# Optimization experiments

Hardware: AMD Instinct MI355X
Metric: run time of the kernel (lower is better)

Reference implementation:

```python
import jax, jax.numpy as jnp
import numpy as np
import math

TAU = 0.5        # module stores self.tau = 1.0 / tau with tau=2.0
THRESHOLD = 1.0
SURR_C = 1.0 / (2.0 * math.sqrt(2.0 * math.pi))  # coefficient in Stochastic.backward


@jax.custom_vjp
def spike(v):
    # Stochastic.forward: (input > 0).float()
    return (v > 0).astype(v.dtype)


def _spike_fwd(v):
    return spike(v), v


def _spike_bwd(v, g):
    # Stochastic.backward: grad * 1/(2*sqrt(2*pi)) * exp(-v^2/2)
    return (g * (SURR_C * jnp.exp(-0.5 * v * v)),)


spike.defvjp(_spike_fwd, _spike_bwd)


def setup_inputs() -> dict:
    key = jax.random.key(0)
    x = jax.random.normal(key, (32, 128, 8192), dtype=jnp.float32)  # [B, T, N]
    return {"x": x}


def reference(x):
    # Eval-mode iterative stochastic-LIF update (no noise injection).
    xt = jnp.swapaxes(x, 0, 1)  # [T, B, N] for scan over time

    def step(u, x_t):
        u = TAU * u + x_t                # leaky integrate
        o = spike(u - THRESHOLD)         # fire
        u = u * (1.0 - o)                # hard reset by multiply
        return u, o

    u0 = jnp.zeros_like(xt[0])
    _, o = jax.lax.scan(step, u0, xt)
    return jnp.swapaxes(o, 0, 1)  # [B, T, N]
```

## Files before the change

kernel.cpp:

```cpp
#include <hip/hip_runtime.h>
#include <stdint.h>


constexpr int B  = 32;
constexpr int T  = 128;
constexpr int N  = 8192;
constexpr int N4 = N / 4;
constexpr int THREADS = 128;
constexpr int SPAN4   = THREADS;
constexpr int NTILES  = N4 / SPAN4;
constexpr int DP      = 16;
constexpr int NG      = T / DP;

typedef float v4f __attribute__((ext_vector_type(4)));

__device__ __forceinline__ float lif1(float& u, float x) {
    u = 0.5f * u + x;
    const bool s = u > 1.0f;
    const float o = s ? 1.0f : 0.0f;
    u = s ? 0.0f : u;
    return o;
}

__device__ __forceinline__ void nt_store4(const float4& o, float4* p) {
    __builtin_nontemporal_store(*(const v4f*)&o, (v4f*)p);
}

__global__ __launch_bounds__(THREADS) void lif_kernel(const float4* __restrict__ x,
                                                      float4* __restrict__ out) {
    const int tid   = threadIdx.x;
    const int b     = blockIdx.x >> 4;
    const int ntile = blockIdx.x & (NTILES - 1);
    const uint32_t base4 = (uint32_t)b * (T * N4) + (uint32_t)ntile * SPAN4 + tid;
    const float4* gx = x + base4;
    float4*       go = out + base4;

    float4 pipe[DP];
    #pragma unroll
    for (int k = 0; k < DP; ++k) pipe[k] = gx[(uint32_t)k * N4];

    float ux = 0.f, uy = 0.f, uz = 0.f, uw = 0.f;

    #pragma unroll 1
    for (int g = 0; g < NG - 1; ++g) {
        const uint32_t roff = (uint32_t)(g + 1) * (DP * N4);
        const uint32_t woff = (uint32_t)g * (DP * N4);
        #pragma unroll
        for (int k = 0; k < DP; ++k) {
            const float4 v = pipe[k];
            pipe[k] = gx[roff + (uint32_t)k * N4];
            float4 o;
            o.x = lif1(ux, v.x);
            o.y = lif1(uy, v.y);
            o.z = lif1(uz, v.z);
            o.w = lif1(uw, v.w);
            nt_store4(o, go + woff + (uint32_t)k * N4);
        }
    }

    {
        const uint32_t woff = (uint32_t)(NG - 1) * (DP * N4);
        #pragma unroll
        for (int k = 0; k < DP; ++k) {
            const float4 v = pipe[k];
            float4 o;
            o.x = lif1(ux, v.x);
            o.y = lif1(uy, v.y);
            o.z = lif1(uz, v.z);
            o.w = lif1(uw, v.w);
            nt_store4(o, go + woff + (uint32_t)k * N4);
        }
    }
}

extern "C" void kernel_launch(void* const* d_in, const int* in_sizes, int n_in,
                              void* d_out, int out_size, void* d_ws, size_t ws_size,
                              hipStream_t stream) {
    const float4* x  = (const float4*)d_in[0];
    float4*      out = (float4*)d_out;
    lif_kernel<<<B * NTILES, THREADS, 0, stream>>>(x, out);
}
```

Baseline: 241.3 us.

## Switch to one neuron per thread with scalar loads for more parallelism

Each thread now handles a single neuron with scalar float loads and stores instead of four neurons via float4. The block size doubles and the grid grows, so four times as many threads run the time recurrence concurrently and the 16-deep prefetch pipe uses fewer registers per thread. This aims to raise occupancy and hide memory latency better, at the cost of narrower memory transactions and more load/store instructions.

```diff
diff --git a/kernel.cpp b/kernel.cpp
--- a/kernel.cpp
+++ b/kernel.cpp
@@ -5,70 +5,53 @@
 constexpr int B  = 32;
 constexpr int T  = 128;
 constexpr int N  = 8192;
-constexpr int N4 = N / 4;
-constexpr int THREADS = 128;
-constexpr int SPAN4   = THREADS;
-constexpr int NTILES  = N4 / SPAN4;
+constexpr int THREADS = 256;
+constexpr int SPAN    = THREADS;
+constexpr int NTILES  = N / SPAN;
 constexpr int DP      = 16;
 constexpr int NG      = T / DP;
 
-typedef float v4f __attribute__((ext_vector_type(4)));
+__global__ __launch_bounds__(THREADS) void lif_kernel(const float* __restrict__ x,
+                                                      float* __restrict__ out) {
+    const int tid   = threadIdx.x;
+    const int b     = blockIdx.x >> 5;
+    const int ntile = blockIdx.x & (NTILES - 1);
+    const uint32_t base = (uint32_t)b * (T * N) + (uint32_t)ntile * SPAN + tid;
+    const float* gx = x + base;
+    float*       go = out + base;
 
-__device__ __forceinline__ float lif1(float& u, float x) {
-    u = 0.5f * u + x;
-    const bool s = u > 1.0f;
-    const float o = s ? 1.0f : 0.0f;
-    u = s ? 0.0f : u;
-    return o;
-}
+    float pipe[DP];
+    #pragma unroll
+    for (int k = 0; k < DP; ++k) pipe[k] = gx[(uint32_t)k * N];
 
-__device__ __forceinline__ void nt_store4(const float4& o, float4* p) {
-    __builtin_nontemporal_store(*(const v4f*)&o, (v4f*)p);
-}
-
-__global__ __launch_bounds__(THREADS) void lif_kernel(const float4* __restrict__ x,
-                                                      float4* __restrict__ out) {
-    const int tid   = threadIdx.x;
-    const int b     = blockIdx.x >> 4;
-    const int ntile = blockIdx.x & (NTILES - 1);
-    const uint32_t base4 = (uint32_t)b * (T * N4) + (uint32_t)ntile * SPAN4 + tid;
-    const float4* gx = x + base4;
-    float4*       go = out + base4;
-
-    float4 pipe[DP];
-    #pragma unroll
-    for (int k = 0; k < DP; ++k) pipe[k] = gx[(uint32_t)k * N4];
-
-    float ux = 0.f, uy = 0.f, uz = 0.f, uw = 0.f;
+    float u = 0.f;
 
     #pragma unroll 1
     for (int g = 0; g < NG - 1; ++g) {
-        const uint32_t roff = (uint32_t)(g + 1) * (DP * N4);
-        const uint32_t woff = (uint32_t)g * (DP * N4);
+        const uint32_t roff = (uint32_t)(g + 1) * (DP * N);
+        const uint32_t woff = (uint32_t)g * (DP * N);
         #pragma unroll
         for (int k = 0; k < DP; ++k) {
-            const float4 v = pipe[k];
-            pipe[k] = gx[roff + (uint32_t)k * N4];
-            float4 o;
-            o.x = lif1(ux, v.x);
-            o.y = lif1(uy, v.y);
-            o.z = lif1(uz, v.z);
-            o.w = lif1(uw, v.w);
-            nt_store4(o, go + woff + (uint32_t)k * N4);
+            const float v = pipe[k];
+            pipe[k] = gx[roff + (uint32_t)k * N];
+            u = 0.5f * u + v;
+            const bool s = u > 1.0f;
+            __builtin_nontemporal_store(s ? 1.0f : 0.0f,
+                                        go + woff + (uint32_t)k * N);
+            u = s ? 0.0f : u;
         }
     }
 
     {
-        const uint32_t woff = (uint32_t)(NG - 1) * (DP * N4);
+        const uint32_t woff = (uint32_t)(NG - 1) * (DP * N);
         #pragma unroll
         for (int k = 0; k < DP; ++k) {
-            const float4 v = pipe[k];
-            float4 o;
-            o.x = lif1(ux, v.x);
-            o.y = lif1(uy, v.y);
-            o.z = lif1(uz, v.z);
-            o.w = lif1(uw, v.w);
-            nt_store4(o, go + woff + (uint32_t)k * N4);
+            const float v = pipe[k];
+            u = 0.5f * u + v;
+            const bool s = u > 1.0f;
+            __builtin_nontemporal_store(s ? 1.0f : 0.0f,
+                                        go + woff + (uint32_t)k * N);
+            u = s ? 0.0f : u;
         }
     }
 }
@@ -76,7 +59,7 @@
 extern "C" void kernel_launch(void* const* d_in, const int* in_sizes, int n_in,
                               void* d_out, int out_size, void* d_ws, size_t ws_size,
                               hipStream_t stream) {
-    const float4* x  = (const float4*)d_in[0];
-    float4*      out = (float4*)d_out;
+    const float* x   = (const float*)d_in[0];
+    float*       out = (float*)d_out;
     lif_kernel<<<B * NTILES, THREADS, 0, stream>>>(x, out);
 }
```

Result: faster. 233.8 us (-3.1%).
